# Kernel optimization log

Measured on AMD Instinct MI355X. Metric: run time of the kernel, lower is better.

Reference implementation:

```python
import jax, jax.numpy as jnp
import numpy as np

N = 200000   # nodes
E = 400000   # edges (edges_0)
G = 4096     # graphs
IN = 63      # in_dim
D = 128      # dim
NG = 6       # num_gaussians


def setup_inputs() -> dict:
    key = jax.random.key(0)
    ks = jax.random.split(key, 10)
    x = jax.random.normal(ks[0], (N, IN), jnp.float32)
    pos = jax.random.normal(ks[1], (N, 3), jnp.float32)
    edges = jax.random.randint(ks[2], (E, 2), 0, N, dtype=jnp.int32).astype(jnp.int64)
    batch = jnp.sort(jax.random.randint(ks[3], (N,), 0, G, dtype=jnp.int32)).astype(jnp.int64)
    # params (xavier-ish scale)
    W = jax.random.normal(ks[4], (IN, D), jnp.float32) * (2.0 / (IN + D)) ** 0.5
    b = jnp.zeros((D,), jnp.float32)
    attn = jax.random.normal(ks[5], (1, D), jnp.float32) * (2.0 / (1 + D)) ** 0.5
    W_rbf = jax.random.normal(ks[6], (NG, D), jnp.float32) * (2.0 / (NG + D)) ** 0.5
    W_read = jax.random.normal(ks[7], (D, 1), jnp.float32) * (2.0 / (D + 1)) ** 0.5
    b_read = jnp.zeros((1,), jnp.float32)
    return dict(x=x, pos=pos, W=W, b=b, attn=attn, W_rbf=W_rbf,
                W_read=W_read, b_read=b_read, edges=edges, batch=batch)


def reference(x, pos, W, b, attn, W_rbf, W_read, b_read, edges, batch):
    # single LineEvoLayer (num_layers=1, dropout=0 -> identity), if_pos=True
    h = x @ W + b                                  # [N, D] (linear computed once)
    src, dst = edges[:, 0], edges[:, 1]
    h_e = jax.nn.elu(h[src] + h[dst])              # [E, D] gather + fuse
    # RBF distance embedding
    vec = pos[dst] - pos[src]                      # [E, 3]
    dist = jnp.maximum(jnp.linalg.norm(vec, axis=1, keepdims=True), 0.1)  # [E, 1]
    offsets = jnp.linspace(0.0, 5.0, NG)           # RBFExpansion(0, 5, 6)
    coeff = -0.5 / (offsets[1] - offsets[0]) ** 2
    rbf = jnp.exp(coeff * (dist - offsets) ** 2)   # [E, NG]
    h_e = h_e * (rbf @ W_rbf)                      # [E, D]
    atom = jax.nn.elu(h_e * attn)                  # [E, D]
    # ReadoutPhase: sigmoid-weighted segment-sum || segment-max over graphs
    eb = batch[src]                                # edge-level graph ids
    score = jax.nn.sigmoid(atom @ W_read + b_read) # [E, 1]
    s_sum = jax.ops.segment_sum(atom * score, eb, num_segments=G)
    s_max = jax.ops.segment_max(atom, eb, num_segments=G)
    s_max = jnp.where(jnp.isfinite(s_max), s_max, 0.0)  # empty segments -> 0
    return jnp.concatenate([s_sum, s_max], axis=1)       # [G, 2*D]
```

## Files before the change

### kernel.cpp

```cpp
#include <hip/hip_runtime.h>
#include <math.h>

constexpr int Nn = 200000, Ee = 400000, Gg = 4096;

__device__ __forceinline__ float elu1(float v) {
    return v > 0.f ? v : __expf(v) - 1.f;
}

__global__ __launch_bounds__(256) void k_zero(int* __restrict__ hist) {
    int i = blockIdx.x * 256 + threadIdx.x;
    if (i < Gg) hist[i] = 0;
}

__global__ __launch_bounds__(256) void k_hist(const int* __restrict__ edges,
                                              const int* __restrict__ batch,
                                              int* __restrict__ hist,
                                              int* __restrict__ ebuf) {
    int e = blockIdx.x * 256 + threadIdx.x;
    if (e >= Ee) return;
    int eb = batch[edges[2 * e]];
    ebuf[e] = eb;
    atomicAdd(&hist[eb], 1);
}

__global__ __launch_bounds__(256) void k_scan(const int* __restrict__ hist,
                                              int* __restrict__ offsets,
                                              int* __restrict__ cursor) {
    __shared__ int part[256];
    int t = threadIdx.x;
    int local[16];
    int s = 0;
#pragma unroll
    for (int j = 0; j < 16; ++j) { local[j] = s; s += hist[t * 16 + j]; }
    part[t] = s;
    __syncthreads();
    for (int off = 1; off < 256; off <<= 1) {
        int v = (t >= off) ? part[t - off] : 0;
        __syncthreads();
        part[t] += v;
        __syncthreads();
    }
    int pre = (t == 0) ? 0 : part[t - 1];
#pragma unroll
    for (int j = 0; j < 16; ++j) {
        int o = pre + local[j];
        offsets[t * 16 + j] = o;
        cursor[t * 16 + j]  = o;
    }
}

__global__ __launch_bounds__(256) void k_scatter(const int* __restrict__ ebuf,
                                                 int* __restrict__ cursor,
                                                 int* __restrict__ order) {
    int e = blockIdx.x * 256 + threadIdx.x;
    if (e >= Ee) return;
    int p = atomicAdd(&cursor[ebuf[e]], 1);
    order[p] = e;
}

__global__ __launch_bounds__(256) void k_pad(const float* __restrict__ x,
                                             float* __restrict__ x64) {
    int total = Nn * 64;
    for (int i = blockIdx.x * 256 + threadIdx.x; i < total; i += gridDim.x * 256) {
        int n = i >> 6, k = i & 63;
        x64[i] = (k < 63) ? x[n * 63 + k] : 0.f;
    }
}

__global__ __launch_bounds__(256, 2) void k_h(const float4* __restrict__ x64q,
                                              const float* __restrict__ W,
                                              const float* __restrict__ b,
                                              float* __restrict__ h, int N) {
    __shared__ float4 xs[2048];
    __shared__ float4 ws[2048];
    int t  = threadIdx.x;
    int tn = t & 15;
    int tm = t >> 4;

    {
        float* wsf = (float*)ws;
        for (int i = t; i < 8192; i += 256) {
            int k = i >> 7, d = i & 127;
            float v  = (k < 63) ? W[k * 128 + d] : 0.f;
            int  pd  = ((d & 7) << 4) | (d >> 3);
            int  kq  = k >> 2, ki = k & 3;
            wsf[(((kq << 7) + ((pd + kq) & 127)) << 2) + ki] = v;
        }
    }
    float bd[8];
#pragma unroll
    for (int i = 0; i < 8; ++i) bd[i] = b[tn * 8 + i];

    int ntiles = (N + 127) >> 7;
    for (int tile = blockIdx.x; tile < ntiles; tile += gridDim.x) {
        int base = tile << 7;
        __syncthreads();
#pragma unroll
        for (int s = 0; s < 8; ++s) {
            int q  = t + s * 256;
            int n  = q >> 4, kq = q & 15;
            int nn = base + n; if (nn > N - 1) nn = N - 1;
            int pn = ((n & 7) << 4) | (n >> 3);
            xs[(kq << 7) + ((pn + kq) & 127)] = x64q[(size_t)nn * 16 + kq];
        }
        __syncthreads();

        float acc[8][8];
#pragma unroll
        for (int j = 0; j < 8; ++j)
#pragma unroll
            for (int i = 0; i < 8; ++i) acc[j][i] = bd[i];

#pragma unroll 2
        for (int kq = 0; kq < 16; ++kq) {
            float4 af[8], bf[8];
#pragma unroll
            for (int j = 0; j < 8; ++j)
                af[j] = xs[(kq << 7) + (((j << 4) + tm + kq) & 127)];
#pragma unroll
            for (int i = 0; i < 8; ++i)
                bf[i] = ws[(kq << 7) + (((i << 4) + tn + kq) & 127)];
#pragma unroll
            for (int j = 0; j < 8; ++j)
#pragma unroll
                for (int i = 0; i < 8; ++i) {
                    acc[j][i] = fmaf(af[j].x, bf[i].x, acc[j][i]);
                    acc[j][i] = fmaf(af[j].y, bf[i].y, acc[j][i]);
                    acc[j][i] = fmaf(af[j].z, bf[i].z, acc[j][i]);
                    acc[j][i] = fmaf(af[j].w, bf[i].w, acc[j][i]);
                }
        }

#pragma unroll
        for (int j = 0; j < 8; ++j) {
            int n = base + tm * 8 + j;
            if (n < N) {
                float4 o0 = {acc[j][0], acc[j][1], acc[j][2], acc[j][3]};
                float4 o1 = {acc[j][4], acc[j][5], acc[j][6], acc[j][7]};
                float4* dst = (float4*)(h + (size_t)n * 128 + tn * 8);
                dst[0] = o0;
                dst[1] = o1;
            }
        }
    }
}

__global__ __launch_bounds__(256) void k_reduce(
    const float* __restrict__ h, const float* __restrict__ pos,
    const float* __restrict__ attn, const float* __restrict__ W_rbf,
    const float* __restrict__ W_read, const float* __restrict__ b_read,
    const int* __restrict__ edges, const int* __restrict__ order,
    const int* __restrict__ offsets, const int* __restrict__ hist,
    float* __restrict__ out) {

    __shared__ float lsum[4][256];
    __shared__ float lmax[4][256];

    int g    = blockIdx.x;
    int t    = threadIdx.x;
    int lane = t & 63;
    int wv   = t >> 6;
    int start = offsets[g];
    int cnt   = hist[g];

    const float2* Wr = (const float2*)W_rbf;
    float2 w0 = Wr[0 * 64 + lane];
    float2 w1 = Wr[1 * 64 + lane];
    float2 w2 = Wr[2 * 64 + lane];
    float2 w3 = Wr[3 * 64 + lane];
    float2 w4 = Wr[4 * 64 + lane];
    float2 w5 = Wr[5 * 64 + lane];
    float2 at = ((const float2*)attn)[lane];
    float2 wr = ((const float2*)W_read)[lane];
    float  br = b_read[0];

    float sx = 0.f, sy = 0.f;
    float mx = -INFINITY, my = -INFINITY;

    for (int i = wv; i < cnt; i += 4) {
        int e   = order[start + i];
        int src = edges[2 * e];
        int dst = edges[2 * e + 1];

        float dx = pos[dst * 3 + 0] - pos[src * 3 + 0];
        float dy = pos[dst * 3 + 1] - pos[src * 3 + 1];
        float dz = pos[dst * 3 + 2] - pos[src * 3 + 2];
        float dist = fmaxf(sqrtf(dx * dx + dy * dy + dz * dz), 0.1f);
        float r0 = __expf(-0.5f * (dist - 0.f) * (dist - 0.f));
        float r1 = __expf(-0.5f * (dist - 1.f) * (dist - 1.f));
        float r2 = __expf(-0.5f * (dist - 2.f) * (dist - 2.f));
        float r3 = __expf(-0.5f * (dist - 3.f) * (dist - 3.f));
        float r4 = __expf(-0.5f * (dist - 4.f) * (dist - 4.f));
        float r5 = __expf(-0.5f * (dist - 5.f) * (dist - 5.f));

        float2 hs = ((const float2*)(h + (size_t)src * 128))[lane];
        float2 hd = ((const float2*)(h + (size_t)dst * 128))[lane];
        float hex = elu1(hs.x + hd.x);
        float hey = elu1(hs.y + hd.y);

        float gx = r0 * w0.x + r1 * w1.x + r2 * w2.x + r3 * w3.x + r4 * w4.x + r5 * w5.x;
        float gy = r0 * w0.y + r1 * w1.y + r2 * w2.y + r3 * w3.y + r4 * w4.y + r5 * w5.y;

        float ax = elu1(hex * gx * at.x);
        float ay = elu1(hey * gy * at.y);

        float p = ax * wr.x + ay * wr.y;
#pragma unroll
        for (int off = 32; off; off >>= 1) p += __shfl_xor(p, off);
        float score = 1.f / (1.f + __expf(-(p + br)));

        sx = fmaf(ax, score, sx);
        sy = fmaf(ay, score, sy);
        mx = fmaxf(mx, ax);
        my = fmaxf(my, ay);
    }

    lsum[wv][lane * 2 + 0] = sx;
    lsum[wv][lane * 2 + 1] = sy;
    lmax[wv][lane * 2 + 0] = mx;
    lmax[wv][lane * 2 + 1] = my;
    __syncthreads();

    float r;
    if (t < 128) {
        r = lsum[0][t] + lsum[1][t] + lsum[2][t] + lsum[3][t];
    } else {
        int d = t - 128;
        float m = fmaxf(fmaxf(lmax[0][d], lmax[1][d]),
                        fmaxf(lmax[2][d], lmax[3][d]));
        r = (m > -3.0e38f) ? m : 0.f;
    }
    out[g * 256 + t] = r;
}

extern "C" void kernel_launch(void* const* d_in, const int* in_sizes, int n_in,
                              void* d_out, int out_size, void* d_ws, size_t ws_size,
                              hipStream_t stream) {
    const float* x      = (const float*)d_in[0];
    const float* pos    = (const float*)d_in[1];
    const float* W      = (const float*)d_in[2];
    const float* b      = (const float*)d_in[3];
    const float* attn   = (const float*)d_in[4];
    const float* W_rbf  = (const float*)d_in[5];
    const float* W_read = (const float*)d_in[6];
    const float* b_read = (const float*)d_in[7];
    const int*   edges  = (const int*)d_in[8];
    const int*   batch  = (const int*)d_in[9];
    float* out = (float*)d_out;

    char* p = (char*)d_ws;
    float* h       = (float*)p;                 p += (size_t)Nn * 128 * 4;
    float* x64     = (float*)p;                 p += (size_t)Nn * 64 * 4;
    int*   hist    = (int*)p;                   p += Gg * 4;
    int*   offsets = (int*)p;                   p += Gg * 4;
    int*   cursor  = (int*)p;                   p += Gg * 4;
    int*   ebuf    = (int*)p;                   p += Ee * 4;
    int*   order   = (int*)p;                   p += Ee * 4;

    k_zero<<<(Gg + 255) / 256, 256, 0, stream>>>(hist);
    k_hist<<<(Ee + 255) / 256, 256, 0, stream>>>(edges, batch, hist, ebuf);
    k_scan<<<1, 256, 0, stream>>>(hist, offsets, cursor);
    k_scatter<<<(Ee + 255) / 256, 256, 0, stream>>>(ebuf, cursor, order);
    k_pad<<<2048, 256, 0, stream>>>(x, x64);
    k_h<<<512, 256, 0, stream>>>((const float4*)x64, W, b, h, Nn);
    k_reduce<<<Gg, 256, 0, stream>>>(h, pos, attn, W_rbf, W_read, b_read,
                                     edges, order, offsets, hist, out);
}
```

Measured before the change: 364.0 us.

## Fuse x padding into GEMM tile load and precompute per-edge RBF values

```diff
diff --git a/kernel.cpp b/kernel.cpp
--- a/kernel.cpp
+++ b/kernel.cpp
@@ -58,16 +58,30 @@
     order[p] = e;
 }
 
-__global__ __launch_bounds__(256) void k_pad(const float* __restrict__ x,
-                                             float* __restrict__ x64) {
-    int total = Nn * 64;
-    for (int i = blockIdx.x * 256 + threadIdx.x; i < total; i += gridDim.x * 256) {
-        int n = i >> 6, k = i & 63;
-        x64[i] = (k < 63) ? x[n * 63 + k] : 0.f;
-    }
-}
-
-__global__ __launch_bounds__(256, 2) void k_h(const float4* __restrict__ x64q,
+__global__ __launch_bounds__(256) void k_rbf(const float* __restrict__ pos,
+                                             const int* __restrict__ edges,
+                                             float4* __restrict__ rbuf) {
+    int e = blockIdx.x * 256 + threadIdx.x;
+    if (e >= Ee) return;
+    int2 ed = ((const int2*)edges)[e];
+    int src = ed.x, dst = ed.y;
+    float dx = pos[dst * 3 + 0] - pos[src * 3 + 0];
+    float dy = pos[dst * 3 + 1] - pos[src * 3 + 1];
+    float dz = pos[dst * 3 + 2] - pos[src * 3 + 2];
+    float dist = fmaxf(sqrtf(dx * dx + dy * dy + dz * dz), 0.1f);
+    float4 a, b4;
+    a.x  = __expf(-0.5f * (dist - 0.f) * (dist - 0.f));
+    a.y  = __expf(-0.5f * (dist - 1.f) * (dist - 1.f));
+    a.z  = __expf(-0.5f * (dist - 2.f) * (dist - 2.f));
+    a.w  = __expf(-0.5f * (dist - 3.f) * (dist - 3.f));
+    b4.x = __expf(-0.5f * (dist - 4.f) * (dist - 4.f));
+    b4.y = __expf(-0.5f * (dist - 5.f) * (dist - 5.f));
+    b4.z = 0.f; b4.w = 0.f;
+    rbuf[2 * e]     = a;
+    rbuf[2 * e + 1] = b4;
+}
+
+__global__ __launch_bounds__(256, 2) void k_h(const float* __restrict__ x,
                                               const float* __restrict__ W,
                                               const float* __restrict__ b,
                                               float* __restrict__ h, int N) {
@@ -76,6 +90,7 @@
     int t  = threadIdx.x;
     int tn = t & 15;
     int tm = t >> 4;
+    float* xsf = (float*)xs;
 
     {
         float* wsf = (float*)ws;
@@ -87,6 +102,10 @@
             wsf[(((kq << 7) + ((pd + kq) & 127)) << 2) + ki] = v;
         }
     }
+    if (t < 128) {
+        int pn = ((t & 7) << 4) | (t >> 3);
+        xsf[(((15 << 7) + ((pn + 15) & 127)) << 2) + 3] = 0.f;
+    }
     float bd[8];
 #pragma unroll
     for (int i = 0; i < 8; ++i) bd[i] = b[tn * 8 + i];
@@ -95,13 +114,17 @@
     for (int tile = blockIdx.x; tile < ntiles; tile += gridDim.x) {
         int base = tile << 7;
         __syncthreads();
-#pragma unroll
-        for (int s = 0; s < 8; ++s) {
-            int q  = t + s * 256;
-            int n  = q >> 4, kq = q & 15;
-            int nn = base + n; if (nn > N - 1) nn = N - 1;
-            int pn = ((n & 7) << 4) | (n >> 3);
-            xs[(kq << 7) + ((pn + kq) & 127)] = x64q[(size_t)nn * 16 + kq];
+        {
+            const float* xg = x + (size_t)base * 63;
+            int lim = Nn * 63 - base * 63;
+            for (int idx = t; idx < 8064; idx += 256) {
+                float v = (idx < lim) ? xg[idx] : 0.f;
+                int n  = idx / 63;
+                int k  = idx - n * 63;
+                int pn = ((n & 7) << 4) | (n >> 3);
+                int kq = k >> 2, ki = k & 3;
+                xsf[(((kq << 7) + ((pn + kq) & 127)) << 2) + ki] = v;
+            }
         }
         __syncthreads();
 
@@ -146,8 +169,9 @@
 }
 
 __global__ __launch_bounds__(256) void k_reduce(
-    const float* __restrict__ h, const float* __restrict__ pos,
-    const float* __restrict__ attn, const float* __restrict__ W_rbf,
+    const float* __restrict__ h, const float4* __restrict__ rbuf,
+    const float* __restrict__ attn,
+    const float* __restrict__ W_rbf,
     const float* __restrict__ W_read, const float* __restrict__ b_read,
     const int* __restrict__ edges, const int* __restrict__ order,
     const int* __restrict__ offsets, const int* __restrict__ hist,
@@ -179,27 +203,19 @@
 
     for (int i = wv; i < cnt; i += 4) {
         int e   = order[start + i];
-        int src = edges[2 * e];
-        int dst = edges[2 * e + 1];
-
-        float dx = pos[dst * 3 + 0] - pos[src * 3 + 0];
-        float dy = pos[dst * 3 + 1] - pos[src * 3 + 1];
-        float dz = pos[dst * 3 + 2] - pos[src * 3 + 2];
-        float dist = fmaxf(sqrtf(dx * dx + dy * dy + dz * dz), 0.1f);
-        float r0 = __expf(-0.5f * (dist - 0.f) * (dist - 0.f));
-        float r1 = __expf(-0.5f * (dist - 1.f) * (dist - 1.f));
-        float r2 = __expf(-0.5f * (dist - 2.f) * (dist - 2.f));
-        float r3 = __expf(-0.5f * (dist - 3.f) * (dist - 3.f));
-        float r4 = __expf(-0.5f * (dist - 4.f) * (dist - 4.f));
-        float r5 = __expf(-0.5f * (dist - 5.f) * (dist - 5.f));
-
-        float2 hs = ((const float2*)(h + (size_t)src * 128))[lane];
-        float2 hd = ((const float2*)(h + (size_t)dst * 128))[lane];
+        int2 ed = ((const int2*)edges)[e];
+        float4 rA = rbuf[2 * e];
+        float4 rB = rbuf[2 * e + 1];
+
+        float2 hs = ((const float2*)(h + (size_t)ed.x * 128))[lane];
+        float2 hd = ((const float2*)(h + (size_t)ed.y * 128))[lane];
         float hex = elu1(hs.x + hd.x);
         float hey = elu1(hs.y + hd.y);
 
-        float gx = r0 * w0.x + r1 * w1.x + r2 * w2.x + r3 * w3.x + r4 * w4.x + r5 * w5.x;
-        float gy = r0 * w0.y + r1 * w1.y + r2 * w2.y + r3 * w3.y + r4 * w4.y + r5 * w5.y;
+        float gx = rA.x * w0.x + rA.y * w1.x + rA.z * w2.x +
+                   rA.w * w3.x + rB.x * w4.x + rB.y * w5.x;
+        float gy = rA.x * w0.y + rA.y * w1.y + rA.z * w2.y +
+                   rA.w * w3.y + rB.x * w4.y + rB.y * w5.y;
 
         float ax = elu1(hex * gx * at.x);
         float ay = elu1(hey * gy * at.y);
@@ -249,20 +265,20 @@
     float* out = (float*)d_out;
 
     char* p = (char*)d_ws;
-    float* h       = (float*)p;                 p += (size_t)Nn * 128 * 4;
-    float* x64     = (float*)p;                 p += (size_t)Nn * 64 * 4;
-    int*   hist    = (int*)p;                   p += Gg * 4;
-    int*   offsets = (int*)p;                   p += Gg * 4;
-    int*   cursor  = (int*)p;                   p += Gg * 4;
-    int*   ebuf    = (int*)p;                   p += Ee * 4;
-    int*   order   = (int*)p;                   p += Ee * 4;
+    float*  h       = (float*)p;                p += (size_t)Nn * 128 * 4;
+    float4* rbuf    = (float4*)p;               p += (size_t)Ee * 32;
+    int*    hist    = (int*)p;                  p += Gg * 4;
+    int*    offsets = (int*)p;                  p += Gg * 4;
+    int*    cursor  = (int*)p;                  p += Gg * 4;
+    int*    ebuf    = (int*)p;                  p += Ee * 4;
+    int*    order   = (int*)p;                  p += Ee * 4;
 
     k_zero<<<(Gg + 255) / 256, 256, 0, stream>>>(hist);
     k_hist<<<(Ee + 255) / 256, 256, 0, stream>>>(edges, batch, hist, ebuf);
     k_scan<<<1, 256, 0, stream>>>(hist, offsets, cursor);
     k_scatter<<<(Ee + 255) / 256, 256, 0, stream>>>(ebuf, cursor, order);
-    k_pad<<<2048, 256, 0, stream>>>(x, x64);
-    k_h<<<512, 256, 0, stream>>>((const float4*)x64, W, b, h, Nn);
-    k_reduce<<<Gg, 256, 0, stream>>>(h, pos, attn, W_rbf, W_read, b_read,
+    k_rbf<<<(Ee + 255) / 256, 256, 0, stream>>>(pos, edges, rbuf);
+    k_h<<<512, 256, 0, stream>>>(x, W, b, h, Nn);
+    k_reduce<<<Gg, 256, 0, stream>>>(h, rbuf, attn, W_rbf, W_read, b_read,
                                      edges, order, offsets, hist, out);
 }
```

New measurement: 374.2 us. 2.8% more time.
